# Kernel optimization log

Measured on AMD Instinct MI355X. Metric: run time of the kernel, lower is better.

Reference implementation:

```python
import jax, jax.numpy as jnp
import numpy as np

D_MODEL = 1024  # scale uses full model dim, as in the source
MASKED = True


def setup_inputs() -> dict:
    key = jax.random.key(0)
    kq, kk, kv = jax.random.split(key, 3)
    B, H, S, Dh = 4, 16, 2048, 64
    Q = jax.random.normal(kq, (B, H, S, Dh), dtype=jnp.float32)
    K = jax.random.normal(kk, (B, H, S, Dh), dtype=jnp.float32)
    V = jax.random.normal(kv, (B, H, S, Dh), dtype=jnp.float32)
    return {"Q": Q, "K": K, "V": V}


def reference(Q, K, V):
    scale = 1.0 / (D_MODEL ** 0.5)
    # [B,H,Sq,Sk] score matrix
    scores = jnp.einsum('bhqd,bhkd->bhqk', Q, K) * scale
    if MASKED:
        S = Q.shape[-2]
        causal = jnp.tril(jnp.ones((S, S), dtype=bool))  # True on/below diag
        scores = jnp.where(causal, scores, jnp.float32(-jnp.inf))
    probs = jax.nn.softmax(scores, axis=-1)
    return jnp.einsum('bhqk,bhkd->bhqd', probs, V)
```

## Files before the change

kernel.cpp:

```cpp
#include <hip/hip_runtime.h>

typedef _Float16 half2_t __attribute__((ext_vector_type(2)));
typedef _Float16 half4_t __attribute__((ext_vector_type(4)));
typedef _Float16 half8_t __attribute__((ext_vector_type(8)));
typedef float    f32x4   __attribute__((ext_vector_type(4)));
typedef unsigned int u32x4 __attribute__((ext_vector_type(4)));

#define S_LEN 2048
#define DH    64
#define QBLK  128
#define KVB   64
#define NQB   16
#define SCALE 0.045110910340389066f

__device__ __forceinline__ int swz_off(int row, int byteInRow) {
    return row * 128 + (byteInRow ^ ((row & 7) << 4));
}

__device__ __forceinline__ half4_t cvt4(f32x4 x) {
    half2_t a = __builtin_bit_cast(half2_t, __builtin_amdgcn_cvt_pkrtz(x[0], x[1]));
    half2_t b = __builtin_bit_cast(half2_t, __builtin_amdgcn_cvt_pkrtz(x[2], x[3]));
    half4_t r; r[0] = a[0]; r[1] = a[1]; r[2] = b[0]; r[3] = b[1];
    return r;
}
__device__ __forceinline__ unsigned int pk2(float a, float b) {
    return __builtin_bit_cast(unsigned int, __builtin_amdgcn_cvt_pkrtz(a, b));
}

__global__ __launch_bounds__(256, 3)
void fattn_kernel(const float* __restrict__ Qg, const float* __restrict__ Kg,
                  const float* __restrict__ Vg, float* __restrict__ Og) {
    __shared__ __align__(16) char smem[32768];

    const int bh  = (int)blockIdx.x;
    const int qb  = (NQB - 1) - (int)blockIdx.y;
    const int q0  = qb * QBLK;
    const int tid = (int)threadIdx.x;
    const int lane = tid & 63;
    const int w    = tid >> 6;
    const int c    = lane & 15;
    const int g    = lane >> 4;

    const size_t base = (size_t)bh * S_LEN * DH;
    const float* Qp = Qg + base;
    const float* Kp = Kg + base;
    const float* Vp = Vg + base;
    float*       Op = Og + base;

    const int qrow = q0 + w * 32;
    const int nT = 2 * qb + 2;

    const bool isK = tid < 128;
    const int sid = tid & 127;
    const int r0  = sid >> 4;
    const int c4  = (sid & 15) << 2;
    const int kLds0 = swz_off(r0, c4 * 2);
    const int s7 = sid >> 4;
    const int ch = s7 >> 2;
    const int qd = s7 & 3;
    const int kbase = 32 * ch + 4 * qd;
    const int d4  = (sid & 15) << 2;
    const int vByte = 64 * ch + 16 * qd;

    half8_t qf[2][2];
#pragma unroll
    for (int qt = 0; qt < 2; ++qt) {
        const float* qptr = Qp + (size_t)(qrow + qt * 16 + c) * DH;
#pragma unroll
        for (int s = 0; s < 2; ++s) {
            f32x4 a = *(const f32x4*)(qptr + s * 32 + g * 8);
            f32x4 b = *(const f32x4*)(qptr + s * 32 + g * 8 + 4);
            half8_t h;
#pragma unroll
            for (int j = 0; j < 4; ++j) {
                h[j]     = (_Float16)(a[j] * SCALE);
                h[j + 4] = (_Float16)(b[j] * SCALE);
            }
            qf[qt][s] = h;
        }
    }

    half8_t ones;
#pragma unroll
    for (int j = 0; j < 8; ++j) ones[j] = (_Float16)1.0f;

    f32x4 oacc0[4], oacc1[4];
#pragma unroll
    for (int dt = 0; dt < 4; ++dt) {
        oacc0[dt] = (f32x4){0.f, 0.f, 0.f, 0.f};
        oacc1[dt] = (f32x4){0.f, 0.f, 0.f, 0.f};
    }
    f32x4 lacc0 = (f32x4){0.f, 0.f, 0.f, 0.f};
    f32x4 lacc1 = (f32x4){0.f, 0.f, 0.f, 0.f};

    f32x4 pr[8];
    auto stage_load = [&](int kv) {
        if (isK) {
#pragma unroll
            for (int i = 0; i < 8; ++i)
                pr[i] = *(const f32x4*)(Kp + (size_t)((kv + r0 + 8 * i) * DH + c4));
        } else {
#pragma unroll
            for (int j = 0; j < 4; ++j) {
                pr[j]     = *(const f32x4*)(Vp + (size_t)((kv + kbase + j) * DH + d4));
                pr[4 + j] = *(const f32x4*)(Vp + (size_t)((kv + kbase + 16 + j) * DH + d4));
            }
        }
    };
    auto stage_write = [&](char* buf) {
        if (isK) {
#pragma unroll
            for (int i = 0; i < 8; ++i)
                *(half4_t*)(buf + kLds0 + i * 1024) = cvt4(pr[i]);
        } else {
            char* Vw = buf + 8192;
#pragma unroll
            for (int jj = 0; jj < 4; ++jj) {
                u32x4 col;
                col[0] = pk2(pr[0][jj], pr[1][jj]);
                col[1] = pk2(pr[2][jj], pr[3][jj]);
                col[2] = pk2(pr[4][jj], pr[5][jj]);
                col[3] = pk2(pr[6][jj], pr[7][jj]);
                *(u32x4*)(Vw + swz_off(d4 + jj, vByte)) = col;
            }
        }
    };

    stage_load(0);
    stage_write(smem);

    int cur = 0;
    for (int t = 0; t < nT; ++t) {
        __syncthreads();
        const bool pf = (t + 1 < nT);
        if (pf) stage_load((t + 1) * KVB);

        const int kv0 = t * KVB;
        char* const Ks = smem + cur * 16384;
        char* const Vs = Ks + 8192;

        if (kv0 <= qrow + 31) {
            f32x4 st0[4], st1[4];
#pragma unroll
            for (int kt = 0; kt < 4; ++kt) {
                st0[kt] = (f32x4){0.f, 0.f, 0.f, 0.f};
                st1[kt] = (f32x4){0.f, 0.f, 0.f, 0.f};
            }
            __builtin_amdgcn_s_setprio(1);
#pragma unroll
            for (int kt = 0; kt < 4; ++kt) {
                half8_t kf0 = *(const half8_t*)(Ks + swz_off(kt * 16 + c, g * 16));
                half8_t kf1 = *(const half8_t*)(Ks + swz_off(kt * 16 + c, 64 + g * 16));
                st0[kt] = __builtin_amdgcn_mfma_f32_16x16x32_f16(kf0, qf[0][0], st0[kt], 0, 0, 0);
                st0[kt] = __builtin_amdgcn_mfma_f32_16x16x32_f16(kf1, qf[0][1], st0[kt], 0, 0, 0);
                st1[kt] = __builtin_amdgcn_mfma_f32_16x16x32_f16(kf0, qf[1][0], st1[kt], 0, 0, 0);
                st1[kt] = __builtin_amdgcn_mfma_f32_16x16x32_f16(kf1, qf[1][1], st1[kt], 0, 0, 0);
            }
            __builtin_amdgcn_s_setprio(0);

            if (kv0 + KVB - 1 > qrow) {
                const int qq0 = qrow + c;
                const int qq1 = qrow + 16 + c;
#pragma unroll
                for (int kt = 0; kt < 4; ++kt)
#pragma unroll
                    for (int r = 0; r < 4; ++r) {
                        const int kk = kv0 + kt * 16 + g * 4 + r;
                        if (kk > qq0) st0[kt][r] = -1e30f;
                        if (kk > qq1) st1[kt][r] = -1e30f;
                    }
            }

            unsigned int pw[8];
#pragma unroll
            for (int kt = 0; kt < 4; ++kt) {
#pragma unroll
                for (int r = 0; r < 4; ++r)
                    st0[kt][r] = __builtin_amdgcn_exp2f(st0[kt][r]);
                pw[2 * kt]     = pk2(st0[kt][0], st0[kt][1]);
                pw[2 * kt + 1] = pk2(st0[kt][2], st0[kt][3]);
            }
            const half8_t phA0 = __builtin_bit_cast(half8_t, (u32x4){pw[0], pw[1], pw[2], pw[3]});
            const half8_t phA1 = __builtin_bit_cast(half8_t, (u32x4){pw[4], pw[5], pw[6], pw[7]});
#pragma unroll
            for (int kt = 0; kt < 4; ++kt) {
#pragma unroll
                for (int r = 0; r < 4; ++r)
                    st1[kt][r] = __builtin_amdgcn_exp2f(st1[kt][r]);
                pw[2 * kt]     = pk2(st1[kt][0], st1[kt][1]);
                pw[2 * kt + 1] = pk2(st1[kt][2], st1[kt][3]);
            }
            const half8_t phB0 = __builtin_bit_cast(half8_t, (u32x4){pw[0], pw[1], pw[2], pw[3]});
            const half8_t phB1 = __builtin_bit_cast(half8_t, (u32x4){pw[4], pw[5], pw[6], pw[7]});

            __builtin_amdgcn_s_setprio(1);
#pragma unroll
            for (int dt = 0; dt < 4; ++dt) {
                half8_t vf = *(const half8_t*)(Vs + swz_off(dt * 16 + c, g * 16));
                oacc0[dt] = __builtin_amdgcn_mfma_f32_16x16x32_f16(vf, phA0, oacc0[dt], 0, 0, 0);
                oacc1[dt] = __builtin_amdgcn_mfma_f32_16x16x32_f16(vf, phB0, oacc1[dt], 0, 0, 0);
            }
            lacc0 = __builtin_amdgcn_mfma_f32_16x16x32_f16(ones, phA0, lacc0, 0, 0, 0);
            lacc1 = __builtin_amdgcn_mfma_f32_16x16x32_f16(ones, phB0, lacc1, 0, 0, 0);
#pragma unroll
            for (int dt = 0; dt < 4; ++dt) {
                half8_t vf = *(const half8_t*)(Vs + swz_off(dt * 16 + c, 64 + g * 16));
                oacc0[dt] = __builtin_amdgcn_mfma_f32_16x16x32_f16(vf, phA1, oacc0[dt], 0, 0, 0);
                oacc1[dt] = __builtin_amdgcn_mfma_f32_16x16x32_f16(vf, phB1, oacc1[dt], 0, 0, 0);
            }
            lacc0 = __builtin_amdgcn_mfma_f32_16x16x32_f16(ones, phA1, lacc0, 0, 0, 0);
            lacc1 = __builtin_amdgcn_mfma_f32_16x16x32_f16(ones, phB1, lacc1, 0, 0, 0);
            __builtin_amdgcn_s_setprio(0);
        }

        if (pf) stage_write(smem + (cur ^ 1) * 16384);
        cur ^= 1;
    }

    {
        const float inv = __builtin_amdgcn_rcpf(lacc0[0]);
        float* optr = Op + (size_t)(qrow + c) * DH;
#pragma unroll
        for (int dt = 0; dt < 4; ++dt) {
            f32x4 o = oacc0[dt] * inv;
            *(f32x4*)(optr + dt * 16 + g * 4) = o;
        }
    }
    {
        const float inv = __builtin_amdgcn_rcpf(lacc1[0]);
        float* optr = Op + (size_t)(qrow + 16 + c) * DH;
#pragma unroll
        for (int dt = 0; dt < 4; ++dt) {
            f32x4 o = oacc1[dt] * inv;
            *(f32x4*)(optr + dt * 16 + g * 4) = o;
        }
    }
}

extern "C" void kernel_launch(void* const* d_in, const int* in_sizes, int n_in,
                              void* d_out, int out_size, void* d_ws, size_t ws_size,
                              hipStream_t stream) {
    (void)in_sizes; (void)n_in; (void)out_size; (void)d_ws; (void)ws_size;
    const float* Q = (const float*)d_in[0];
    const float* K = (const float*)d_in[1];
    const float* V = (const float*)d_in[2];
    float* O = (float*)d_out;
    dim3 grid(64, NQB);
    fattn_kernel<<<grid, 256, 0, stream>>>(Q, K, V, O);
}
```

Measured before the change: 54.27 us.

## Shrink Q and KV tiles to 64x32 with two-wave blocks and padded V layout

After: 69.28 us. +27.7%, slower.

```diff
diff --git a/kernel.cpp b/kernel.cpp
--- a/kernel.cpp
+++ b/kernel.cpp
@@ -1,36 +1,30 @@
 #include <hip/hip_runtime.h>
 
 typedef _Float16 half2_t __attribute__((ext_vector_type(2)));
-typedef _Float16 half4_t __attribute__((ext_vector_type(4)));
 typedef _Float16 half8_t __attribute__((ext_vector_type(8)));
 typedef float    f32x4   __attribute__((ext_vector_type(4)));
 typedef unsigned int u32x4 __attribute__((ext_vector_type(4)));
 
 #define S_LEN 2048
 #define DH    64
-#define QBLK  128
-#define KVB   64
-#define NQB   16
+#define QBLK  64
+#define KVB   32
+#define NQB   32
 #define SCALE 0.045110910340389066f
 
+#define VROW   80
+#define BUFSZ  9216
 __device__ __forceinline__ int swz_off(int row, int byteInRow) {
     return row * 128 + (byteInRow ^ ((row & 7) << 4));
 }
-
-__device__ __forceinline__ half4_t cvt4(f32x4 x) {
-    half2_t a = __builtin_bit_cast(half2_t, __builtin_amdgcn_cvt_pkrtz(x[0], x[1]));
-    half2_t b = __builtin_bit_cast(half2_t, __builtin_amdgcn_cvt_pkrtz(x[2], x[3]));
-    half4_t r; r[0] = a[0]; r[1] = a[1]; r[2] = b[0]; r[3] = b[1];
-    return r;
-}
 __device__ __forceinline__ unsigned int pk2(float a, float b) {
     return __builtin_bit_cast(unsigned int, __builtin_amdgcn_cvt_pkrtz(a, b));
 }
 
-__global__ __launch_bounds__(256, 3)
+__global__ __launch_bounds__(128, 4)
 void fattn_kernel(const float* __restrict__ Qg, const float* __restrict__ Kg,
                   const float* __restrict__ Vg, float* __restrict__ Og) {
-    __shared__ __align__(16) char smem[32768];
+    __shared__ __align__(16) char smem[2 * BUFSZ];
 
     const int bh  = (int)blockIdx.x;
     const int qb  = (NQB - 1) - (int)blockIdx.y;
@@ -48,19 +42,15 @@
     float*       Op = Og + base;
 
     const int qrow = q0 + w * 32;
-    const int nT = 2 * qb + 2;
-
-    const bool isK = tid < 128;
-    const int sid = tid & 127;
-    const int r0  = sid >> 4;
-    const int c4  = (sid & 15) << 2;
-    const int kLds0 = swz_off(r0, c4 * 2);
-    const int s7 = sid >> 4;
-    const int ch = s7 >> 2;
-    const int qd = s7 & 3;
-    const int kbase = 32 * ch + 4 * qd;
+    const int nT = qb + 1;
+    const int nT2 = 2 * qb + 2;
+
+    const bool isK = (w == 0);
+    const int sid = lane;
+    const int r0  = sid >> 3;
+    const int c8  = (sid & 7) << 3;
+    const int qd  = sid >> 4;
     const int d4  = (sid & 15) << 2;
-    const int vByte = 64 * ch + 16 * qd;
 
     half8_t qf[2][2];
 #pragma unroll
@@ -97,23 +87,31 @@
     auto stage_load = [&](int kv) {
         if (isK) {
 #pragma unroll
-            for (int i = 0; i < 8; ++i)
-                pr[i] = *(const f32x4*)(Kp + (size_t)((kv + r0 + 8 * i) * DH + c4));
+            for (int i = 0; i < 4; ++i) {
+                pr[2*i]   = *(const f32x4*)(Kp + (size_t)((kv + r0 + 8*i) * DH + c8));
+                pr[2*i+1] = *(const f32x4*)(Kp + (size_t)((kv + r0 + 8*i) * DH + c8 + 4));
+            }
         } else {
 #pragma unroll
             for (int j = 0; j < 4; ++j) {
-                pr[j]     = *(const f32x4*)(Vp + (size_t)((kv + kbase + j) * DH + d4));
-                pr[4 + j] = *(const f32x4*)(Vp + (size_t)((kv + kbase + 16 + j) * DH + d4));
+                pr[j]     = *(const f32x4*)(Vp + (size_t)((kv + 4*qd + j) * DH + d4));
+                pr[4 + j] = *(const f32x4*)(Vp + (size_t)((kv + 16 + 4*qd + j) * DH + d4));
             }
         }
     };
     auto stage_write = [&](char* buf) {
         if (isK) {
 #pragma unroll
-            for (int i = 0; i < 8; ++i)
-                *(half4_t*)(buf + kLds0 + i * 1024) = cvt4(pr[i]);
+            for (int i = 0; i < 4; ++i) {
+                u32x4 kw;
+                kw[0] = pk2(pr[2*i][0],   pr[2*i][1]);
+                kw[1] = pk2(pr[2*i][2],   pr[2*i][3]);
+                kw[2] = pk2(pr[2*i+1][0], pr[2*i+1][1]);
+                kw[3] = pk2(pr[2*i+1][2], pr[2*i+1][3]);
+                *(u32x4*)(buf + swz_off(r0 + 8*i, c8 * 2)) = kw;
+            }
         } else {
-            char* Vw = buf + 8192;
+            char* Vw = buf + 4096;
 #pragma unroll
             for (int jj = 0; jj < 4; ++jj) {
                 u32x4 col;
@@ -121,7 +119,7 @@
                 col[1] = pk2(pr[2][jj], pr[3][jj]);
                 col[2] = pk2(pr[4][jj], pr[5][jj]);
                 col[3] = pk2(pr[6][jj], pr[7][jj]);
-                *(u32x4*)(Vw + swz_off(d4 + jj, vByte)) = col;
+                *(u32x4*)(Vw + (d4 + jj) * VROW + 16 * qd) = col;
             }
         }
     };
@@ -130,25 +128,25 @@
     stage_write(smem);
 
     int cur = 0;
-    for (int t = 0; t < nT; ++t) {
+    for (int t = 0; t < nT2; ++t) {
         __syncthreads();
-        const bool pf = (t + 1 < nT);
+        const bool pf = (t + 1 < nT2);
         if (pf) stage_load((t + 1) * KVB);
 
         const int kv0 = t * KVB;
-        char* const Ks = smem + cur * 16384;
-        char* const Vs = Ks + 8192;
+        char* const Ks = smem + cur * BUFSZ;
+        char* const Vs = Ks + 4096;
 
         if (kv0 <= qrow + 31) {
-            f32x4 st0[4], st1[4];
-#pragma unroll
-            for (int kt = 0; kt < 4; ++kt) {
+            f32x4 st0[2], st1[2];
+#pragma unroll
+            for (int kt = 0; kt < 2; ++kt) {
                 st0[kt] = (f32x4){0.f, 0.f, 0.f, 0.f};
                 st1[kt] = (f32x4){0.f, 0.f, 0.f, 0.f};
             }
             __builtin_amdgcn_s_setprio(1);
 #pragma unroll
-            for (int kt = 0; kt < 4; ++kt) {
+            for (int kt = 0; kt < 2; ++kt) {
                 half8_t kf0 = *(const half8_t*)(Ks + swz_off(kt * 16 + c, g * 16));
                 half8_t kf1 = *(const half8_t*)(Ks + swz_off(kt * 16 + c, 64 + g * 16));
                 st0[kt] = __builtin_amdgcn_mfma_f32_16x16x32_f16(kf0, qf[0][0], st0[kt], 0, 0, 0);
@@ -162,7 +160,7 @@
                 const int qq0 = qrow + c;
                 const int qq1 = qrow + 16 + c;
 #pragma unroll
-                for (int kt = 0; kt < 4; ++kt)
+                for (int kt = 0; kt < 2; ++kt)
 #pragma unroll
                     for (int r = 0; r < 4; ++r) {
                         const int kk = kv0 + kt * 16 + g * 4 + r;
@@ -171,49 +169,34 @@
                     }
             }
 
-            unsigned int pw[8];
-#pragma unroll
-            for (int kt = 0; kt < 4; ++kt) {
-#pragma unroll
-                for (int r = 0; r < 4; ++r)
+#pragma unroll
+            for (int kt = 0; kt < 2; ++kt)
+#pragma unroll
+                for (int r = 0; r < 4; ++r) {
                     st0[kt][r] = __builtin_amdgcn_exp2f(st0[kt][r]);
-                pw[2 * kt]     = pk2(st0[kt][0], st0[kt][1]);
-                pw[2 * kt + 1] = pk2(st0[kt][2], st0[kt][3]);
-            }
-            const half8_t phA0 = __builtin_bit_cast(half8_t, (u32x4){pw[0], pw[1], pw[2], pw[3]});
-            const half8_t phA1 = __builtin_bit_cast(half8_t, (u32x4){pw[4], pw[5], pw[6], pw[7]});
-#pragma unroll
-            for (int kt = 0; kt < 4; ++kt) {
-#pragma unroll
-                for (int r = 0; r < 4; ++r)
                     st1[kt][r] = __builtin_amdgcn_exp2f(st1[kt][r]);
-                pw[2 * kt]     = pk2(st1[kt][0], st1[kt][1]);
-                pw[2 * kt + 1] = pk2(st1[kt][2], st1[kt][3]);
-            }
-            const half8_t phB0 = __builtin_bit_cast(half8_t, (u32x4){pw[0], pw[1], pw[2], pw[3]});
-            const half8_t phB1 = __builtin_bit_cast(half8_t, (u32x4){pw[4], pw[5], pw[6], pw[7]});
+                }
+            u32x4 pa, pb;
+            pa[0] = pk2(st0[0][0], st0[0][1]); pa[1] = pk2(st0[0][2], st0[0][3]);
+            pa[2] = pk2(st0[1][0], st0[1][1]); pa[3] = pk2(st0[1][2], st0[1][3]);
+            pb[0] = pk2(st1[0][0], st1[0][1]); pb[1] = pk2(st1[0][2], st1[0][3]);
+            pb[2] = pk2(st1[1][0], st1[1][1]); pb[3] = pk2(st1[1][2], st1[1][3]);
+            const half8_t phA = __builtin_bit_cast(half8_t, pa);
+            const half8_t phB = __builtin_bit_cast(half8_t, pb);
 
             __builtin_amdgcn_s_setprio(1);
 #pragma unroll
             for (int dt = 0; dt < 4; ++dt) {
-                half8_t vf = *(const half8_t*)(Vs + swz_off(dt * 16 + c, g * 16));
-                oacc0[dt] = __builtin_amdgcn_mfma_f32_16x16x32_f16(vf, phA0, oacc0[dt], 0, 0, 0);
-                oacc1[dt] = __builtin_amdgcn_mfma_f32_16x16x32_f16(vf, phB0, oacc1[dt], 0, 0, 0);
-            }
-            lacc0 = __builtin_amdgcn_mfma_f32_16x16x32_f16(ones, phA0, lacc0, 0, 0, 0);
-            lacc1 = __builtin_amdgcn_mfma_f32_16x16x32_f16(ones, phB0, lacc1, 0, 0, 0);
-#pragma unroll
-            for (int dt = 0; dt < 4; ++dt) {
-                half8_t vf = *(const half8_t*)(Vs + swz_off(dt * 16 + c, 64 + g * 16));
-                oacc0[dt] = __builtin_amdgcn_mfma_f32_16x16x32_f16(vf, phA1, oacc0[dt], 0, 0, 0);
-                oacc1[dt] = __builtin_amdgcn_mfma_f32_16x16x32_f16(vf, phB1, oacc1[dt], 0, 0, 0);
-            }
-            lacc0 = __builtin_amdgcn_mfma_f32_16x16x32_f16(ones, phA1, lacc0, 0, 0, 0);
-            lacc1 = __builtin_amdgcn_mfma_f32_16x16x32_f16(ones, phB1, lacc1, 0, 0, 0);
+                half8_t vf = *(const half8_t*)(Vs + (dt * 16 + c) * VROW + g * 16);
+                oacc0[dt] = __builtin_amdgcn_mfma_f32_16x16x32_f16(vf, phA, oacc0[dt], 0, 0, 0);
+                oacc1[dt] = __builtin_amdgcn_mfma_f32_16x16x32_f16(vf, phB, oacc1[dt], 0, 0, 0);
+            }
+            lacc0 = __builtin_amdgcn_mfma_f32_16x16x32_f16(ones, phA, lacc0, 0, 0, 0);
+            lacc1 = __builtin_amdgcn_mfma_f32_16x16x32_f16(ones, phB, lacc1, 0, 0, 0);
             __builtin_amdgcn_s_setprio(0);
         }
 
-        if (pf) stage_write(smem + (cur ^ 1) * 16384);
+        if (pf) stage_write(smem + (cur ^ 1) * BUFSZ);
         cur ^= 1;
     }
 
@@ -246,5 +229,5 @@
     const float* V = (const float*)d_in[2];
     float* O = (float*)d_out;
     dim3 grid(64, NQB);
-    fattn_kernel<<<grid, 256, 0, stream>>>(Q, K, V, O);
-}
+    fattn_kernel<<<grid, 128, 0, stream>>>(Q, K, V, O);
+}
```

## Process 128-key KV tiles per barrier with two 64-key half bodies

Applied to the files above, without the earlier changes.

Result: slower. 67.52 us (+24.4%).

```diff
diff --git a/kernel.cpp b/kernel.cpp
--- a/kernel.cpp
+++ b/kernel.cpp
@@ -9,7 +9,7 @@
 #define S_LEN 2048
 #define DH    64
 #define QBLK  128
-#define KVB   64
+#define KVB   128
 #define NQB   16
 #define SCALE 0.045110910340389066f
 
@@ -30,7 +30,7 @@
 __global__ __launch_bounds__(256, 3)
 void fattn_kernel(const float* __restrict__ Qg, const float* __restrict__ Kg,
                   const float* __restrict__ Vg, float* __restrict__ Og) {
-    __shared__ __align__(16) char smem[32768];
+    __shared__ __align__(16) char smem[65536];
 
     const int bh  = (int)blockIdx.x;
     const int qb  = (NQB - 1) - (int)blockIdx.y;
@@ -48,7 +48,7 @@
     float*       Op = Og + base;
 
     const int qrow = q0 + w * 32;
-    const int nT = 2 * qb + 2;
+    const int nT = qb + 1;
 
     const bool isK = tid < 128;
     const int sid = tid & 127;
@@ -107,13 +107,12 @@
             }
         }
     };
-    auto stage_write = [&](char* buf) {
+    auto stage_write = [&](char* Kb, char* Vb) {
         if (isK) {
 #pragma unroll
             for (int i = 0; i < 8; ++i)
-                *(half4_t*)(buf + kLds0 + i * 1024) = cvt4(pr[i]);
+                *(half4_t*)(Kb + kLds0 + i * 1024) = cvt4(pr[i]);
         } else {
-            char* Vw = buf + 8192;
 #pragma unroll
             for (int jj = 0; jj < 4; ++jj) {
                 u32x4 col;
@@ -121,99 +120,112 @@
                 col[1] = pk2(pr[2][jj], pr[3][jj]);
                 col[2] = pk2(pr[4][jj], pr[5][jj]);
                 col[3] = pk2(pr[6][jj], pr[7][jj]);
-                *(u32x4*)(Vw + swz_off(d4 + jj, vByte)) = col;
+                *(u32x4*)(Vb + swz_off(d4 + jj, vByte)) = col;
             }
         }
     };
 
+    auto half_body = [&](const char* Ksh, const char* Vsh, int kv0h) {
+        f32x4 st0[4], st1[4];
+#pragma unroll
+        for (int kt = 0; kt < 4; ++kt) {
+            st0[kt] = (f32x4){0.f, 0.f, 0.f, 0.f};
+            st1[kt] = (f32x4){0.f, 0.f, 0.f, 0.f};
+        }
+        __builtin_amdgcn_s_setprio(1);
+#pragma unroll
+        for (int kt = 0; kt < 4; ++kt) {
+            half8_t kf0 = *(const half8_t*)(Ksh + swz_off(kt * 16 + c, g * 16));
+            half8_t kf1 = *(const half8_t*)(Ksh + swz_off(kt * 16 + c, 64 + g * 16));
+            st0[kt] = __builtin_amdgcn_mfma_f32_16x16x32_f16(kf0, qf[0][0], st0[kt], 0, 0, 0);
+            st0[kt] = __builtin_amdgcn_mfma_f32_16x16x32_f16(kf1, qf[0][1], st0[kt], 0, 0, 0);
+            st1[kt] = __builtin_amdgcn_mfma_f32_16x16x32_f16(kf0, qf[1][0], st1[kt], 0, 0, 0);
+            st1[kt] = __builtin_amdgcn_mfma_f32_16x16x32_f16(kf1, qf[1][1], st1[kt], 0, 0, 0);
+        }
+        __builtin_amdgcn_s_setprio(0);
+
+        if (kv0h + 63 > qrow) {
+            const int qq0 = qrow + c;
+            const int qq1 = qrow + 16 + c;
+#pragma unroll
+            for (int kt = 0; kt < 4; ++kt)
+#pragma unroll
+                for (int r = 0; r < 4; ++r) {
+                    const int kk = kv0h + kt * 16 + g * 4 + r;
+                    if (kk > qq0) st0[kt][r] = -1e30f;
+                    if (kk > qq1) st1[kt][r] = -1e30f;
+                }
+        }
+
+        unsigned int pw[8];
+#pragma unroll
+        for (int kt = 0; kt < 4; ++kt) {
+#pragma unroll
+            for (int r = 0; r < 4; ++r)
+                st0[kt][r] = __builtin_amdgcn_exp2f(st0[kt][r]);
+            pw[2 * kt]     = pk2(st0[kt][0], st0[kt][1]);
+            pw[2 * kt + 1] = pk2(st0[kt][2], st0[kt][3]);
+        }
+        const half8_t phA0 = __builtin_bit_cast(half8_t, (u32x4){pw[0], pw[1], pw[2], pw[3]});
+        const half8_t phA1 = __builtin_bit_cast(half8_t, (u32x4){pw[4], pw[5], pw[6], pw[7]});
+#pragma unroll
+        for (int kt = 0; kt < 4; ++kt) {
+#pragma unroll
+            for (int r = 0; r < 4; ++r)
+                st1[kt][r] = __builtin_amdgcn_exp2f(st1[kt][r]);
+            pw[2 * kt]     = pk2(st1[kt][0], st1[kt][1]);
+            pw[2 * kt + 1] = pk2(st1[kt][2], st1[kt][3]);
+        }
+        const half8_t phB0 = __builtin_bit_cast(half8_t, (u32x4){pw[0], pw[1], pw[2], pw[3]});
+        const half8_t phB1 = __builtin_bit_cast(half8_t, (u32x4){pw[4], pw[5], pw[6], pw[7]});
+
+        __builtin_amdgcn_s_setprio(1);
+#pragma unroll
+        for (int dt = 0; dt < 4; ++dt) {
+            half8_t vf = *(const half8_t*)(Vsh + swz_off(dt * 16 + c, g * 16));
+            oacc0[dt] = __builtin_amdgcn_mfma_f32_16x16x32_f16(vf, phA0, oacc0[dt], 0, 0, 0);
+            oacc1[dt] = __builtin_amdgcn_mfma_f32_16x16x32_f16(vf, phB0, oacc1[dt], 0, 0, 0);
+        }
+        lacc0 = __builtin_amdgcn_mfma_f32_16x16x32_f16(ones, phA0, lacc0, 0, 0, 0);
+        lacc1 = __builtin_amdgcn_mfma_f32_16x16x32_f16(ones, phB0, lacc1, 0, 0, 0);
+#pragma unroll
+        for (int dt = 0; dt < 4; ++dt) {
+            half8_t vf = *(const half8_t*)(Vsh + swz_off(dt * 16 + c, 64 + g * 16));
+            oacc0[dt] = __builtin_amdgcn_mfma_f32_16x16x32_f16(vf, phA1, oacc0[dt], 0, 0, 0);
+            oacc1[dt] = __builtin_amdgcn_mfma_f32_16x16x32_f16(vf, phB1, oacc1[dt], 0, 0, 0);
+        }
+        lacc0 = __builtin_amdgcn_mfma_f32_16x16x32_f16(ones, phA1, lacc0, 0, 0, 0);
+        lacc1 = __builtin_amdgcn_mfma_f32_16x16x32_f16(ones, phB1, lacc1, 0, 0, 0);
+        __builtin_amdgcn_s_setprio(0);
+    };
+
     stage_load(0);
-    stage_write(smem);
+    stage_write(smem, smem + 16384);
+    stage_load(64);
+    stage_write(smem + 8192, smem + 24576);
 
     int cur = 0;
     for (int t = 0; t < nT; ++t) {
         __syncthreads();
         const bool pf = (t + 1 < nT);
+        const int kv0 = t * KVB;
+        char* const B  = smem + cur * 32768;
+        char* const Bn = smem + (cur ^ 1) * 32768;
+
         if (pf) stage_load((t + 1) * KVB);
 
-        const int kv0 = t * KVB;
-        char* const Ks = smem + cur * 16384;
-        char* const Vs = Ks + 8192;
-
-        if (kv0 <= qrow + 31) {
-            f32x4 st0[4], st1[4];
-#pragma unroll
-            for (int kt = 0; kt < 4; ++kt) {
-                st0[kt] = (f32x4){0.f, 0.f, 0.f, 0.f};
-                st1[kt] = (f32x4){0.f, 0.f, 0.f, 0.f};
-            }
-            __builtin_amdgcn_s_setprio(1);
-#pragma unroll
-            for (int kt = 0; kt < 4; ++kt) {
-                half8_t kf0 = *(const half8_t*)(Ks + swz_off(kt * 16 + c, g * 16));
-                half8_t kf1 = *(const half8_t*)(Ks + swz_off(kt * 16 + c, 64 + g * 16));
-                st0[kt] = __builtin_amdgcn_mfma_f32_16x16x32_f16(kf0, qf[0][0], st0[kt], 0, 0, 0);
-                st0[kt] = __builtin_amdgcn_mfma_f32_16x16x32_f16(kf1, qf[0][1], st0[kt], 0, 0, 0);
-                st1[kt] = __builtin_amdgcn_mfma_f32_16x16x32_f16(kf0, qf[1][0], st1[kt], 0, 0, 0);
-                st1[kt] = __builtin_amdgcn_mfma_f32_16x16x32_f16(kf1, qf[1][1], st1[kt], 0, 0, 0);
-            }
-            __builtin_amdgcn_s_setprio(0);
-
-            if (kv0 + KVB - 1 > qrow) {
-                const int qq0 = qrow + c;
-                const int qq1 = qrow + 16 + c;
-#pragma unroll
-                for (int kt = 0; kt < 4; ++kt)
-#pragma unroll
-                    for (int r = 0; r < 4; ++r) {
-                        const int kk = kv0 + kt * 16 + g * 4 + r;
-                        if (kk > qq0) st0[kt][r] = -1e30f;
-                        if (kk > qq1) st1[kt][r] = -1e30f;
-                    }
-            }
-
-            unsigned int pw[8];
-#pragma unroll
-            for (int kt = 0; kt < 4; ++kt) {
-#pragma unroll
-                for (int r = 0; r < 4; ++r)
-                    st0[kt][r] = __builtin_amdgcn_exp2f(st0[kt][r]);
-                pw[2 * kt]     = pk2(st0[kt][0], st0[kt][1]);
-                pw[2 * kt + 1] = pk2(st0[kt][2], st0[kt][3]);
-            }
-            const half8_t phA0 = __builtin_bit_cast(half8_t, (u32x4){pw[0], pw[1], pw[2], pw[3]});
-            const half8_t phA1 = __builtin_bit_cast(half8_t, (u32x4){pw[4], pw[5], pw[6], pw[7]});
-#pragma unroll
-            for (int kt = 0; kt < 4; ++kt) {
-#pragma unroll
-                for (int r = 0; r < 4; ++r)
-                    st1[kt][r] = __builtin_amdgcn_exp2f(st1[kt][r]);
-                pw[2 * kt]     = pk2(st1[kt][0], st1[kt][1]);
-                pw[2 * kt + 1] = pk2(st1[kt][2], st1[kt][3]);
-            }
-            const half8_t phB0 = __builtin_bit_cast(half8_t, (u32x4){pw[0], pw[1], pw[2], pw[3]});
-            const half8_t phB1 = __builtin_bit_cast(half8_t, (u32x4){pw[4], pw[5], pw[6], pw[7]});
-
-            __builtin_amdgcn_s_setprio(1);
-#pragma unroll
-            for (int dt = 0; dt < 4; ++dt) {
-                half8_t vf = *(const half8_t*)(Vs + swz_off(dt * 16 + c, g * 16));
-                oacc0[dt] = __builtin_amdgcn_mfma_f32_16x16x32_f16(vf, phA0, oacc0[dt], 0, 0, 0);
-                oacc1[dt] = __builtin_amdgcn_mfma_f32_16x16x32_f16(vf, phB0, oacc1[dt], 0, 0, 0);
-            }
-            lacc0 = __builtin_amdgcn_mfma_f32_16x16x32_f16(ones, phA0, lacc0, 0, 0, 0);
-            lacc1 = __builtin_amdgcn_mfma_f32_16x16x32_f16(ones, phB0, lacc1, 0, 0, 0);
-#pragma unroll
-            for (int dt = 0; dt < 4; ++dt) {
-                half8_t vf = *(const half8_t*)(Vs + swz_off(dt * 16 + c, 64 + g * 16));
-                oacc0[dt] = __builtin_amdgcn_mfma_f32_16x16x32_f16(vf, phA1, oacc0[dt], 0, 0, 0);
-                oacc1[dt] = __builtin_amdgcn_mfma_f32_16x16x32_f16(vf, phB1, oacc1[dt], 0, 0, 0);
-            }
-            lacc0 = __builtin_amdgcn_mfma_f32_16x16x32_f16(ones, phA1, lacc0, 0, 0, 0);
-            lacc1 = __builtin_amdgcn_mfma_f32_16x16x32_f16(ones, phB1, lacc1, 0, 0, 0);
-            __builtin_amdgcn_s_setprio(0);
-        }
-
-        if (pf) stage_write(smem + (cur ^ 1) * 16384);
+        half_body(B, B + 16384, kv0);
+
+        if (pf) {
+            stage_write(Bn, Bn + 16384);
+            stage_load((t + 1) * KVB + 64);
+        }
+
+        if (kv0 + 64 <= qrow + 31) {
+            half_body(B + 8192, B + 24576, kv0 + 64);
+        }
+
+        if (pf) stage_write(Bn + 8192, Bn + 24576);
         cur ^= 1;
     }
 
```

## Use 2 waves per block with 64 query rows each and split staging

Applied to the files above, without the earlier changes.

Result: slower. 70.61 us (+30.1%).

```diff
diff --git a/kernel.cpp b/kernel.cpp
--- a/kernel.cpp
+++ b/kernel.cpp
@@ -1,7 +1,6 @@
 #include <hip/hip_runtime.h>
 
 typedef _Float16 half2_t __attribute__((ext_vector_type(2)));
-typedef _Float16 half4_t __attribute__((ext_vector_type(4)));
 typedef _Float16 half8_t __attribute__((ext_vector_type(8)));
 typedef float    f32x4   __attribute__((ext_vector_type(4)));
 typedef unsigned int u32x4 __attribute__((ext_vector_type(4)));
@@ -16,18 +15,11 @@
 __device__ __forceinline__ int swz_off(int row, int byteInRow) {
     return row * 128 + (byteInRow ^ ((row & 7) << 4));
 }
-
-__device__ __forceinline__ half4_t cvt4(f32x4 x) {
-    half2_t a = __builtin_bit_cast(half2_t, __builtin_amdgcn_cvt_pkrtz(x[0], x[1]));
-    half2_t b = __builtin_bit_cast(half2_t, __builtin_amdgcn_cvt_pkrtz(x[2], x[3]));
-    half4_t r; r[0] = a[0]; r[1] = a[1]; r[2] = b[0]; r[3] = b[1];
-    return r;
-}
 __device__ __forceinline__ unsigned int pk2(float a, float b) {
     return __builtin_bit_cast(unsigned int, __builtin_amdgcn_cvt_pkrtz(a, b));
 }
 
-__global__ __launch_bounds__(256, 3)
+__global__ __launch_bounds__(128, 2)
 void fattn_kernel(const float* __restrict__ Qg, const float* __restrict__ Kg,
                   const float* __restrict__ Vg, float* __restrict__ Og) {
     __shared__ __align__(16) char smem[32768];
@@ -47,36 +39,35 @@
     const float* Vp = Vg + base;
     float*       Op = Og + base;
 
-    const int qrow = q0 + w * 32;
+    const int qrow = q0 + w * 64;
     const int nT = 2 * qb + 2;
 
-    const bool isK = tid < 128;
-    const int sid = tid & 127;
-    const int r0  = sid >> 4;
-    const int c4  = (sid & 15) << 2;
-    const int kLds0 = swz_off(r0, c4 * 2);
-    const int s7 = sid >> 4;
-    const int ch = s7 >> 2;
-    const int qd = s7 & 3;
-    const int kbase = 32 * ch + 4 * qd;
+    const bool isK = tid < 64;
+    const int sid = tid & 63;
+    const int r0  = sid >> 3;
+    const int u8  = sid & 7;
+    const int c8  = u8 << 3;
+    const int kByte = u8 << 4;
     const int d4  = (sid & 15) << 2;
-    const int vByte = 64 * ch + 16 * qd;
-
-    half8_t qf[2][2];
-#pragma unroll
-    for (int qt = 0; qt < 2; ++qt) {
-        const float* qptr = Qp + (size_t)(qrow + qt * 16 + c) * DH;
-#pragma unroll
-        for (int s = 0; s < 2; ++s) {
-            f32x4 a = *(const f32x4*)(qptr + s * 32 + g * 8);
-            f32x4 b = *(const f32x4*)(qptr + s * 32 + g * 8 + 4);
-            half8_t h;
+    const int u   = sid >> 4;
+    const int ch  = u >> 1;
+    const int qd2 = (u & 1) << 1;
+
+    half8_t qf[4][2];
+#pragma unroll
+    for (int s = 0; s < 4; ++s) {
+        const float* qptr = Qp + (size_t)(qrow + s * 16 + c) * DH;
+#pragma unroll
+        for (int h = 0; h < 2; ++h) {
+            f32x4 a = *(const f32x4*)(qptr + h * 32 + g * 8);
+            f32x4 b = *(const f32x4*)(qptr + h * 32 + g * 8 + 4);
+            half8_t hh;
 #pragma unroll
             for (int j = 0; j < 4; ++j) {
-                h[j]     = (_Float16)(a[j] * SCALE);
-                h[j + 4] = (_Float16)(b[j] * SCALE);
-            }
-            qf[qt][s] = h;
+                hh[j]     = (_Float16)(a[j] * SCALE);
+                hh[j + 4] = (_Float16)(b[j] * SCALE);
+            }
+            qf[s][h] = hh;
         }
     }
 
@@ -84,22 +75,26 @@
 #pragma unroll
     for (int j = 0; j < 8; ++j) ones[j] = (_Float16)1.0f;
 
-    f32x4 oacc0[4], oacc1[4];
-#pragma unroll
-    for (int dt = 0; dt < 4; ++dt) {
-        oacc0[dt] = (f32x4){0.f, 0.f, 0.f, 0.f};
-        oacc1[dt] = (f32x4){0.f, 0.f, 0.f, 0.f};
-    }
-    f32x4 lacc0 = (f32x4){0.f, 0.f, 0.f, 0.f};
-    f32x4 lacc1 = (f32x4){0.f, 0.f, 0.f, 0.f};
+    f32x4 oacc[4][4];
+    f32x4 lacc[4];
+#pragma unroll
+    for (int s = 0; s < 4; ++s) {
+        lacc[s] = (f32x4){0.f, 0.f, 0.f, 0.f};
+#pragma unroll
+        for (int dt = 0; dt < 4; ++dt) oacc[s][dt] = (f32x4){0.f, 0.f, 0.f, 0.f};
+    }
 
     f32x4 pr[8];
-    auto stage_load = [&](int kv) {
+    auto stage_load = [&](int kv, int p) {
         if (isK) {
 #pragma unroll
-            for (int i = 0; i < 8; ++i)
-                pr[i] = *(const f32x4*)(Kp + (size_t)((kv + r0 + 8 * i) * DH + c4));
+            for (int i = 0; i < 4; ++i) {
+                const int row = r0 + 8 * (i + 4 * p);
+                pr[2*i]   = *(const f32x4*)(Kp + (size_t)((kv + row) * DH + c8));
+                pr[2*i+1] = *(const f32x4*)(Kp + (size_t)((kv + row) * DH + c8 + 4));
+            }
         } else {
+            const int kbase = 32 * ch + 4 * (qd2 + p);
 #pragma unroll
             for (int j = 0; j < 4; ++j) {
                 pr[j]     = *(const f32x4*)(Vp + (size_t)((kv + kbase + j) * DH + d4));
@@ -107,13 +102,21 @@
             }
         }
     };
-    auto stage_write = [&](char* buf) {
+    auto stage_write = [&](char* buf, int p) {
         if (isK) {
 #pragma unroll
-            for (int i = 0; i < 8; ++i)
-                *(half4_t*)(buf + kLds0 + i * 1024) = cvt4(pr[i]);
+            for (int i = 0; i < 4; ++i) {
+                const int row = r0 + 8 * (i + 4 * p);
+                u32x4 kw;
+                kw[0] = pk2(pr[2*i][0],   pr[2*i][1]);
+                kw[1] = pk2(pr[2*i][2],   pr[2*i][3]);
+                kw[2] = pk2(pr[2*i+1][0], pr[2*i+1][1]);
+                kw[3] = pk2(pr[2*i+1][2], pr[2*i+1][3]);
+                *(u32x4*)(buf + swz_off(row, kByte)) = kw;
+            }
         } else {
             char* Vw = buf + 8192;
+            const int vByte = 64 * ch + 16 * (qd2 + p);
 #pragma unroll
             for (int jj = 0; jj < 4; ++jj) {
                 u32x4 col;
@@ -126,112 +129,112 @@
         }
     };
 
-    stage_load(0);
-    stage_write(smem);
+    stage_load(0, 0);
+    stage_write(smem, 0);
+    stage_load(0, 1);
+    stage_write(smem, 1);
 
     int cur = 0;
     for (int t = 0; t < nT; ++t) {
         __syncthreads();
         const bool pf = (t + 1 < nT);
-        if (pf) stage_load((t + 1) * KVB);
+        if (pf) stage_load((t + 1) * KVB, 0);
 
         const int kv0 = t * KVB;
         char* const Ks = smem + cur * 16384;
         char* const Vs = Ks + 8192;
-
-        if (kv0 <= qrow + 31) {
-            f32x4 st0[4], st1[4];
-#pragma unroll
-            for (int kt = 0; kt < 4; ++kt) {
-                st0[kt] = (f32x4){0.f, 0.f, 0.f, 0.f};
-                st1[kt] = (f32x4){0.f, 0.f, 0.f, 0.f};
-            }
+        const bool live = (kv0 <= qrow + 63);
+
+        f32x4 st[4][4];
+        half8_t ph[4][2];
+        if (live) {
+#pragma unroll
+            for (int s = 0; s < 4; ++s)
+#pragma unroll
+                for (int kt = 0; kt < 4; ++kt)
+                    st[s][kt] = (f32x4){0.f, 0.f, 0.f, 0.f};
             __builtin_amdgcn_s_setprio(1);
 #pragma unroll
             for (int kt = 0; kt < 4; ++kt) {
                 half8_t kf0 = *(const half8_t*)(Ks + swz_off(kt * 16 + c, g * 16));
                 half8_t kf1 = *(const half8_t*)(Ks + swz_off(kt * 16 + c, 64 + g * 16));
-                st0[kt] = __builtin_amdgcn_mfma_f32_16x16x32_f16(kf0, qf[0][0], st0[kt], 0, 0, 0);
-                st0[kt] = __builtin_amdgcn_mfma_f32_16x16x32_f16(kf1, qf[0][1], st0[kt], 0, 0, 0);
-                st1[kt] = __builtin_amdgcn_mfma_f32_16x16x32_f16(kf0, qf[1][0], st1[kt], 0, 0, 0);
-                st1[kt] = __builtin_amdgcn_mfma_f32_16x16x32_f16(kf1, qf[1][1], st1[kt], 0, 0, 0);
+#pragma unroll
+                for (int s = 0; s < 4; ++s) {
+                    st[s][kt] = __builtin_amdgcn_mfma_f32_16x16x32_f16(kf0, qf[s][0], st[s][kt], 0, 0, 0);
+                    st[s][kt] = __builtin_amdgcn_mfma_f32_16x16x32_f16(kf1, qf[s][1], st[s][kt], 0, 0, 0);
+                }
             }
             __builtin_amdgcn_s_setprio(0);
 
-            if (kv0 + KVB - 1 > qrow) {
-                const int qq0 = qrow + c;
-                const int qq1 = qrow + 16 + c;
-#pragma unroll
-                for (int kt = 0; kt < 4; ++kt)
-#pragma unroll
-                    for (int r = 0; r < 4; ++r) {
-                        const int kk = kv0 + kt * 16 + g * 4 + r;
-                        if (kk > qq0) st0[kt][r] = -1e30f;
-                        if (kk > qq1) st1[kt][r] = -1e30f;
-                    }
-            }
-
-            unsigned int pw[8];
-#pragma unroll
-            for (int kt = 0; kt < 4; ++kt) {
-#pragma unroll
-                for (int r = 0; r < 4; ++r)
-                    st0[kt][r] = __builtin_amdgcn_exp2f(st0[kt][r]);
-                pw[2 * kt]     = pk2(st0[kt][0], st0[kt][1]);
-                pw[2 * kt + 1] = pk2(st0[kt][2], st0[kt][3]);
-            }
-            const half8_t phA0 = __builtin_bit_cast(half8_t, (u32x4){pw[0], pw[1], pw[2], pw[3]});
-            const half8_t phA1 = __builtin_bit_cast(half8_t, (u32x4){pw[4], pw[5], pw[6], pw[7]});
-#pragma unroll
-            for (int kt = 0; kt < 4; ++kt) {
-#pragma unroll
-                for (int r = 0; r < 4; ++r)
-                    st1[kt][r] = __builtin_amdgcn_exp2f(st1[kt][r]);
-                pw[2 * kt]     = pk2(st1[kt][0], st1[kt][1]);
-                pw[2 * kt + 1] = pk2(st1[kt][2], st1[kt][3]);
-            }
-            const half8_t phB0 = __builtin_bit_cast(half8_t, (u32x4){pw[0], pw[1], pw[2], pw[3]});
-            const half8_t phB1 = __builtin_bit_cast(half8_t, (u32x4){pw[4], pw[5], pw[6], pw[7]});
-
+            if (kv0 + 63 > qrow) {
+#pragma unroll
+                for (int s = 0; s < 4; ++s) {
+                    const int qq = qrow + 16 * s + c;
+#pragma unroll
+                    for (int kt = 0; kt < 4; ++kt)
+#pragma unroll
+                        for (int r = 0; r < 4; ++r)
+                            if (kv0 + kt * 16 + g * 4 + r > qq) st[s][kt][r] = -1e30f;
+                }
+            }
+
+#pragma unroll
+            for (int s = 0; s < 4; ++s) {
+                unsigned int pw[8];
+#pragma unroll
+                for (int kt = 0; kt < 4; ++kt) {
+#pragma unroll
+                    for (int r = 0; r < 4; ++r)
+                        st[s][kt][r] = __builtin_amdgcn_exp2f(st[s][kt][r]);
+                    pw[2 * kt]     = pk2(st[s][kt][0], st[s][kt][1]);
+                    pw[2 * kt + 1] = pk2(st[s][kt][2], st[s][kt][3]);
+                }
+                ph[s][0] = __builtin_bit_cast(half8_t, (u32x4){pw[0], pw[1], pw[2], pw[3]});
+                ph[s][1] = __builtin_bit_cast(half8_t, (u32x4){pw[4], pw[5], pw[6], pw[7]});
+            }
+        }
+
+        if (pf) {
+            stage_write(smem + (cur ^ 1) * 16384, 0);
+            stage_load((t + 1) * KVB, 1);
+        }
+
+        if (live) {
             __builtin_amdgcn_s_setprio(1);
 #pragma unroll
             for (int dt = 0; dt < 4; ++dt) {
                 half8_t vf = *(const half8_t*)(Vs + swz_off(dt * 16 + c, g * 16));
-                oacc0[dt] = __builtin_amdgcn_mfma_f32_16x16x32_f16(vf, phA0, oacc0[dt], 0, 0, 0);
-                oacc1[dt] = __builtin_amdgcn_mfma_f32_16x16x32_f16(vf, phB0, oacc1[dt], 0, 0, 0);
-            }
-            lacc0 = __builtin_amdgcn_mfma_f32_16x16x32_f16(ones, phA0, lacc0, 0, 0, 0);
-            lacc1 = __builtin_amdgcn_mfma_f32_16x16x32_f16(ones, phB0, lacc1, 0, 0, 0);
+#pragma unroll
+                for (int s = 0; s < 4; ++s)
+                    oacc[s][dt] = __builtin_amdgcn_mfma_f32_16x16x32_f16(vf, ph[s][0], oacc[s][dt], 0, 0, 0);
+            }
+#pragma unroll
+            for (int s = 0; s < 4; ++s)
+                lacc[s] = __builtin_amdgcn_mfma_f32_16x16x32_f16(ones, ph[s][0], lacc[s], 0, 0, 0);
 #pragma unroll
             for (int dt = 0; dt < 4; ++dt) {
                 half8_t vf = *(const half8_t*)(Vs + swz_off(dt * 16 + c, 64 + g * 16));
-                oacc0[dt] = __builtin_amdgcn_mfma_f32_16x16x32_f16(vf, phA1, oacc0[dt], 0, 0, 0);
-                oacc1[dt] = __builtin_amdgcn_mfma_f32_16x16x32_f16(vf, phB1, oacc1[dt], 0, 0, 0);
-            }
-            lacc0 = __builtin_amdgcn_mfma_f32_16x16x32_f16(ones, phA1, lacc0, 0, 0, 0);
-            lacc1 = __builtin_amdgcn_mfma_f32_16x16x32_f16(ones, phB1, lacc1, 0, 0, 0);
+#pragma unroll
+                for (int s = 0; s < 4; ++s)
+                    oacc[s][dt] = __builtin_amdgcn_mfma_f32_16x16x32_f16(vf, ph[s][1], oacc[s][dt], 0, 0, 0);
+            }
+#pragma unroll
+            for (int s = 0; s < 4; ++s)
+                lacc[s] = __builtin_amdgcn_mfma_f32_16x16x32_f16(ones, ph[s][1], lacc[s], 0, 0, 0);
             __builtin_amdgcn_s_setprio(0);
         }
 
-        if (pf) stage_write(smem + (cur ^ 1) * 16384);
+        if (pf) stage_write(smem + (cur ^ 1) * 16384, 1);
         cur ^= 1;
     }
 
-    {
-        const float inv = __builtin_amdgcn_rcpf(lacc0[0]);
-        float* optr = Op + (size_t)(qrow + c) * DH;
+#pragma unroll
+    for (int s = 0; s < 4; ++s) {
+        const float inv = __builtin_amdgcn_rcpf(lacc[s][0]);
+        float* optr = Op + (size_t)(qrow + 16 * s + c) * DH;
 #pragma unroll
         for (int dt = 0; dt < 4; ++dt) {
-            f32x4 o = oacc0[dt] * inv;
-            *(f32x4*)(optr + dt * 16 + g * 4) = o;
-        }
-    }
-    {
-        const float inv = __builtin_amdgcn_rcpf(lacc1[0]);
-        float* optr = Op + (size_t)(qrow + 16 + c) * DH;
-#pragma unroll
-        for (int dt = 0; dt < 4; ++dt) {
-            f32x4 o = oacc1[dt] * inv;
+            f32x4 o = oacc[s][dt] * inv;
             *(f32x4*)(optr + dt * 16 + g * 4) = o;
         }
     }
@@ -246,5 +249,5 @@
     const float* V = (const float*)d_in[2];
     float* O = (float*)d_out;
     dim3 grid(64, NQB);
-    fattn_kernel<<<grid, 256, 0, stream>>>(Q, K, V, O);
-}
+    fattn_kernel<<<grid, 128, 0, stream>>>(Q, K, V, O);
+}
```
